# Optimization experiments

Measured on AMD Instinct MI355X. Metric: run time of the kernel, lower is better.

## Reference

```python
import jax, jax.numpy as jnp
import numpy as np

B, S, H = 2, 2048, 1024
G, HEADS = 4, 16
HPG = HEADS // G          # heads per group = 4
HD = H // HEADS           # head_dim = 64
DG = H // G               # per-group proj dim = 256
SCALE = 1.0 / np.sqrt(HD)


def setup_inputs() -> dict:
    key = jax.random.key(0)
    ks = jax.random.split(key, 6)
    w = 0.02
    return {
        "hidden_states": jax.random.normal(ks[0], (B, S, H), dtype=jnp.float32),
        "Wq": jax.random.normal(ks[1], (G, DG, H), dtype=jnp.float32) * w,
        "bq": jnp.zeros((G, DG), dtype=jnp.float32),
        "Wk": jax.random.normal(ks[2], (G, DG, H), dtype=jnp.float32) * w,
        "bk": jnp.zeros((G, DG), dtype=jnp.float32),
        "Wv": jax.random.normal(ks[3], (G, DG, H), dtype=jnp.float32) * w,
        "bv": jnp.zeros((G, DG), dtype=jnp.float32),
        "Wo": jax.random.normal(ks[4], (H, H), dtype=jnp.float32) * w,
        "bo": jnp.zeros((H,), dtype=jnp.float32),
    }


def _proj_split(x, W, b):
    # x: [B,S,H], W: [G,DG,H], b: [G,DG] -> [B,G,HPG,S,HD]
    y = jnp.einsum("bsh,gdh->bgsd", x, W) + b[None, :, None, :]
    y = y.reshape(x.shape[0], G, x.shape[1], HPG, HD)
    return jnp.transpose(y, (0, 1, 3, 2, 4))


def reference(hidden_states, Wq, bq, Wk, bk, Wv, bv, Wo, bo):
    q = _proj_split(hidden_states, Wq, bq)  # [B,G,HPG,S,HD]
    k = _proj_split(hidden_states, Wk, bk)
    v = _proj_split(hidden_states, Wv, bv)
    scores = jnp.einsum("bghqd,bghkd->bghqk", q, k) * SCALE
    attn = jax.nn.softmax(scores.astype(jnp.float32), axis=-1).astype(v.dtype)
    ctx = jnp.einsum("bghqk,bghkd->bghqd", attn, v)  # [B,G,HPG,S,HD]
    # merge: heads ordered group-major, matching torch cat over group dim
    ctx = jnp.transpose(ctx, (0, 3, 1, 2, 4)).reshape(hidden_states.shape[0], hidden_states.shape[1], H)
    return jnp.einsum("bsh,oh->bso", ctx, Wo) + bo
```

## Files before the change

### kernel.cpp

```cpp
#include <hip/hip_runtime.h>

typedef __bf16 bf16x8 __attribute__((ext_vector_type(8)));
typedef float f32x4 __attribute__((ext_vector_type(4)));
typedef float f32x16 __attribute__((ext_vector_type(16)));
typedef unsigned int uint4v __attribute__((ext_vector_type(4)));
typedef unsigned int uint2v __attribute__((ext_vector_type(2)));

#define LOG2E 1.4426950408889634f

static __device__ __forceinline__ unsigned short f2bf(float f) {
  union { float f; unsigned int u; } c; c.f = f;
  return (unsigned short)((c.u + 0x7fffu + ((c.u >> 16) & 1u)) >> 16);
}

static __device__ __forceinline__ void gload16(const void* g, void* l) {
  __builtin_amdgcn_global_load_lds(
      (const __attribute__((address_space(1))) void*)g,
      (__attribute__((address_space(3))) void*)l, 16, 0, 0);
}

static __device__ __forceinline__ float exp2fast(float x) {
#if __has_builtin(__builtin_amdgcn_exp2f)
  return __builtin_amdgcn_exp2f(x);
#else
  return exp2f(x);
#endif
}

static __device__ __forceinline__ f32x16 mfma32(bf16x8 a, bf16x8 b, f32x16 c) {
  return __builtin_amdgcn_mfma_f32_32x32x16_bf16(a, b, c, 0, 0, 0);
}

static __device__ __forceinline__ unsigned cvt_pk_bf16(float a, float b) {
  unsigned r;
  asm("v_cvt_pk_bf16_f32 %0, %1, %2" : "=v"(r) : "v"(a), "v"(b));
  return r;
}

static __device__ __forceinline__ void pl32_swap(unsigned& a, unsigned& b) {
#if __has_builtin(__builtin_amdgcn_permlane32_swap)
  uint2v r = __builtin_amdgcn_permlane32_swap(a, b, false, false);
  a = r[0]; b = r[1];
#else
  asm volatile("v_permlane32_swap_b32 %0, %1" : "+v"(a), "+v"(b));
#endif
}

__global__ void cvt_all(const float* __restrict__ x,
                        const float* __restrict__ Wq,
                        const float* __restrict__ Wk,
                        const float* __restrict__ Wv,
                        const float* __restrict__ Wo,
                        ushort4* __restrict__ dst) {
  int i = blockIdx.x * 256 + threadIdx.x;
  const float* src;
  int off;
  if (i < 1048576) {
    src = x; off = i;
  } else {
    int t = (i - 1048576) >> 18;
    off = (i - 1048576) & 262143;
    src = (t == 0) ? Wq : (t == 1) ? Wk : (t == 2) ? Wv : Wo;
  }
  float4 f = ((const float4*)src)[off];
  ushort4 o;
  o.x = f2bf(f.x); o.y = f2bf(f.y); o.z = f2bf(f.z); o.w = f2bf(f.w);
  dst[i] = o;
}

__launch_bounds__(256, 4)
__global__ void qkv_gemm(const unsigned short* __restrict__ xb,
                         const unsigned short* __restrict__ wq,
                         const unsigned short* __restrict__ wk,
                         const unsigned short* __restrict__ wv,
                         const float* __restrict__ bq,
                         const float* __restrict__ bk,
                         const float* __restrict__ bv,
                         unsigned short* __restrict__ Qo,
                         unsigned short* __restrict__ Ko,
                         unsigned short* __restrict__ VTo) {
  __shared__ unsigned short As[128 * 64];
  __shared__ unsigned short Bs[128 * 64];
  const int lg = (blockIdx.x & 7) * 96 + (blockIdx.x >> 3);
  const int s0 = (lg & 31) * 128;
  const int n0g = (lg >> 5) * 128;
  const int qkv = n0g >> 10;
  const int d0 = n0g & 1023;
  const unsigned short* W = (qkv == 0) ? wq : ((qkv == 1) ? wk : wv);
  const float* bias = (qkv == 0) ? bq : ((qkv == 1) ? bk : bv);

  const unsigned short* Aptr; const unsigned short* Bptr;
  int Aoff, Boff;
  if (qkv < 2) { Aptr = W;  Aoff = d0; Bptr = xb; Boff = s0; }
  else         { Aptr = xb; Aoff = s0; Bptr = W;  Boff = d0; }

  const int tid = threadIdx.x;
  const int lane = tid & 63;
  const int wid = tid >> 6;
  const int wm = (wid >> 1) * 64;
  const int wn = (wid & 1) * 64;
  const int lm = lane & 15;
  const int quad = lane >> 4;

  f32x4 acc[4][4] = {};

  for (int kk = 0; kk < 1024; kk += 64) {
#pragma unroll
    for (int t = 0; t < 4; ++t) {
      int i = t * 256 + tid;
      int row = i >> 3, tp = i & 7;
      int seg = tp ^ (row & 7);
      gload16(Aptr + (size_t)(Aoff + row) * 1024 + kk + seg * 8,
              As + (size_t)i * 8);
      gload16(Bptr + (size_t)(Boff + row) * 1024 + kk + seg * 8,
              Bs + (size_t)i * 8);
    }
    __syncthreads();
#pragma unroll
    for (int h = 0; h < 2; ++h) {
      bf16x8 af[4], bff[4];
#pragma unroll
      for (int mt = 0; mt < 4; ++mt) {
        int r = wm + mt * 16 + lm;
        af[mt] = *(const bf16x8*)(As + r * 64 + (((h * 4 + quad) ^ (r & 7)) * 8));
      }
#pragma unroll
      for (int nt = 0; nt < 4; ++nt) {
        int r = wn + nt * 16 + lm;
        bff[nt] = *(const bf16x8*)(Bs + r * 64 + (((h * 4 + quad) ^ (r & 7)) * 8));
      }
#pragma unroll
      for (int mt = 0; mt < 4; ++mt)
#pragma unroll
        for (int nt = 0; nt < 4; ++nt)
          acc[mt][nt] = __builtin_amdgcn_mfma_f32_16x16x32_bf16(
              af[mt], bff[nt], acc[mt][nt], 0, 0, 0);
    }
    __syncthreads();
  }

  if (qkv < 2) {
    unsigned short* OUT = (qkv == 0) ? Qo : Ko;
    const float scale = (qkv == 0) ? (0.125f * LOG2E) : 1.0f;
#pragma unroll
    for (int mt = 0; mt < 4; ++mt) {
      const int d = d0 + wm + mt * 16 + quad * 4;
      const int g = d >> 8, hpg = (d >> 6) & 3, hd = d & 63;
      const float4 bb = *(const float4*)(bias + d);
#pragma unroll
      for (int nt = 0; nt < 4; ++nt) {
        const int srow = s0 + wn + nt * 16 + lm;
        const int bidx = srow >> 11, s = srow & 2047;
        const int head = (bidx * 4 + g) * 4 + hpg;
        ushort4 o;
        o.x = f2bf((acc[mt][nt][0] + bb.x) * scale);
        o.y = f2bf((acc[mt][nt][1] + bb.y) * scale);
        o.z = f2bf((acc[mt][nt][2] + bb.z) * scale);
        o.w = f2bf((acc[mt][nt][3] + bb.w) * scale);
        *(ushort4*)(OUT + (size_t)head * 131072 + (size_t)s * 64 + hd) = o;
      }
    }
  } else {
#pragma unroll
    for (int nt = 0; nt < 4; ++nt) {
      const int d = d0 + wn + nt * 16 + lm;
      const int g = d >> 8, hpg = (d >> 6) & 3, hd = d & 63;
      const float bb = bias[d];
#pragma unroll
      for (int mt = 0; mt < 4; ++mt) {
        const int sbase = s0 + wm + mt * 16 + quad * 4;
        const int bidx = sbase >> 11, s = sbase & 2047;
        const int head = (bidx * 4 + g) * 4 + hpg;
        ushort4 o;
        o.x = f2bf(acc[mt][nt][0] + bb);
        o.y = f2bf(acc[mt][nt][1] + bb);
        o.z = f2bf(acc[mt][nt][2] + bb);
        o.w = f2bf(acc[mt][nt][3] + bb);
        *(ushort4*)(VTo + (size_t)head * 131072 + (size_t)hd * 2048 + s) = o;
      }
    }
  }
}

static __device__ __forceinline__ void stage_kv(
    const unsigned short* Kh, const unsigned short* Vh, int kv0,
    unsigned short* ksl, unsigned short* vsl, int tid) {
#pragma unroll
  for (int t = 0; t < 4; ++t) {
    int i = t * 256 + tid;
    int r = i >> 3, j = i & 7;
    gload16(Kh + (size_t)(kv0 + r) * 64 + ((j ^ (r & 7)) << 3),
            ksl + (size_t)i * 8);
  }
#pragma unroll
  for (int t = 0; t < 4; ++t) {
    int i = t * 256 + tid;
    int r = i >> 4, j = i & 15;
    gload16(Vh + (size_t)r * 2048 + kv0 + ((j ^ (r & 15)) << 3),
            vsl + (size_t)i * 8);
  }
}

__launch_bounds__(256, 2)
__global__ void attn_kernel(const unsigned short* __restrict__ Q,
                            const unsigned short* __restrict__ K,
                            const unsigned short* __restrict__ VT,
                            unsigned short* __restrict__ ctx) {
  __shared__ __align__(16) unsigned char smem[65536];

  const int f = blockIdx.x;
  const int xcd = f & 7;
  const int idx = f >> 3;
  const int head = xcd * 4 + (idx & 3);
  const int q0 = (idx >> 2) * 128;
  const int b = head >> 4;
  const int colbase = (head & 15) * 64;

  const unsigned short* Qh = Q + (size_t)head * 131072;
  const unsigned short* Kh = K + (size_t)head * 131072;
  const unsigned short* Vh = VT + (size_t)head * 131072;

  const int tid = threadIdx.x;
  const int lane = tid & 63;
  const int w = tid >> 6;
  const int wq = w & 1;
  const int wkv = w >> 1;
  const int l31 = lane & 31;
  const int hi = lane >> 5;

  stage_kv(Kh, Vh, 0, (unsigned short*)smem,
           (unsigned short*)(smem + 32768), tid);

  bf16x8 qf[2][4];
#pragma unroll
  for (int qs = 0; qs < 2; ++qs) {
    const size_t qrow = (size_t)(q0 + wq * 64 + qs * 32 + l31);
#pragma unroll
    for (int s = 0; s < 4; ++s)
      qf[qs][s] = *(const bf16x8*)(Qh + qrow * 64 + s * 16 + hi * 8);
  }

  int koff[2][4];
#pragma unroll
  for (int kb = 0; kb < 2; ++kb) {
    const int row = wkv * 64 + kb * 32 + l31;
#pragma unroll
    for (int s = 0; s < 4; ++s) {
      const int c = s * 2 + hi;
      koff[kb][s] = row * 64 + ((c ^ (row & 7)) << 3);
    }
  }
  int voff[2][2][2];
#pragma unroll
  for (int kb = 0; kb < 2; ++kb)
#pragma unroll
    for (int db = 0; db < 2; ++db) {
      const int row = db * 32 + l31;
#pragma unroll
      for (int t = 0; t < 2; ++t) {
        const int c = wkv * 8 + kb * 4 + t * 2 + hi;
        voff[kb][db][t] = row * 128 + ((c ^ (row & 15)) << 3);
      }
    }

  __syncthreads();

  float psum[2] = {0.f, 0.f};
  f32x16 oacc[2][2] = {};

  for (int it = 0; it < 16; ++it) {
    const int buf = it & 1;
    const unsigned short* kbuf = (const unsigned short*)(smem + buf * 16384);
    const unsigned short* vbuf =
        (const unsigned short*)(smem + 32768 + buf * 16384);
    if (it < 15)
      stage_kv(Kh, Vh, (it + 1) * 128,
               (unsigned short*)(smem + (buf ^ 1) * 16384),
               (unsigned short*)(smem + 32768 + (buf ^ 1) * 16384), tid);

#pragma unroll
    for (int kb = 0; kb < 2; ++kb) {
      bf16x8 kf[4], vf[2][2];
#pragma unroll
      for (int s = 0; s < 4; ++s)
        kf[s] = *(const bf16x8*)(kbuf + koff[kb][s]);
#pragma unroll
      for (int db = 0; db < 2; ++db)
#pragma unroll
        for (int t = 0; t < 2; ++t)
          vf[db][t] = *(const bf16x8*)(vbuf + voff[kb][db][t]);

#pragma unroll
      for (int qs = 0; qs < 2; ++qs) {
        f32x16 sc = {};
#pragma unroll
        for (int s = 0; s < 4; ++s)
          sc = mfma32(kf[s], qf[qs][s], sc);

        float e[16];
#pragma unroll
        for (int r = 0; r < 16; ++r) e[r] = exp2fast(sc[r]);
        {
          float t0 = (e[0] + e[1]) + (e[2] + e[3]);
          float t1 = (e[4] + e[5]) + (e[6] + e[7]);
          float t2 = (e[8] + e[9]) + (e[10] + e[11]);
          float t3 = (e[12] + e[13]) + (e[14] + e[15]);
          psum[qs] += (t0 + t1) + (t2 + t3);
        }
        unsigned p[8];
#pragma unroll
        for (int j = 0; j < 8; ++j) p[j] = cvt_pk_bf16(e[2 * j], e[2 * j + 1]);
        pl32_swap(p[0], p[2]); pl32_swap(p[1], p[3]);
        pl32_swap(p[4], p[6]); pl32_swap(p[5], p[7]);
        uint4v u0 = {p[0], p[1], p[2], p[3]};
        uint4v u1 = {p[4], p[5], p[6], p[7]};
        const bf16x8 B0 = __builtin_bit_cast(bf16x8, u0);
        const bf16x8 B1 = __builtin_bit_cast(bf16x8, u1);
#pragma unroll
        for (int db = 0; db < 2; ++db) {
          oacc[qs][db] = mfma32(vf[db][0], B0, oacc[qs][db]);
          oacc[qs][db] = mfma32(vf[db][1], B1, oacc[qs][db]);
        }
      }
    }
    __syncthreads();
  }

#pragma unroll
  for (int qs = 0; qs < 2; ++qs)
    psum[qs] += __shfl_xor(psum[qs], 32, 64);

  float* red = (float*)smem;
  float* psred = (float*)(smem + 34816);
  if (wkv == 1) {
#pragma unroll
    for (int qs = 0; qs < 2; ++qs) {
      const int qi = wq * 64 + qs * 32 + l31;
      if (hi == 0) psred[qi] = psum[qs];
#pragma unroll
      for (int db = 0; db < 2; ++db)
#pragma unroll
        for (int g = 0; g < 4; ++g) {
          f32x4 ov;
          ov[0] = oacc[qs][db][4 * g + 0];
          ov[1] = oacc[qs][db][4 * g + 1];
          ov[2] = oacc[qs][db][4 * g + 2];
          ov[3] = oacc[qs][db][4 * g + 3];
          *(f32x4*)(red + qi * 68 + db * 32 + g * 8 + hi * 4) = ov;
        }
    }
  }
  __syncthreads();
  if (wkv == 0) {
#pragma unroll
    for (int qs = 0; qs < 2; ++qs) {
      const int qi = wq * 64 + qs * 32 + l31;
      const float inv = 1.0f / (psum[qs] + psred[qi]);
      const size_t row = (size_t)(b * 2048 + q0 + qi);
#pragma unroll
      for (int db = 0; db < 2; ++db)
#pragma unroll
        for (int g = 0; g < 4; ++g) {
          f32x4 o = *(const f32x4*)(red + qi * 68 + db * 32 + g * 8 + hi * 4);
          ushort4 st;
          st.x = f2bf((o[0] + oacc[qs][db][4 * g + 0]) * inv);
          st.y = f2bf((o[1] + oacc[qs][db][4 * g + 1]) * inv);
          st.z = f2bf((o[2] + oacc[qs][db][4 * g + 2]) * inv);
          st.w = f2bf((o[3] + oacc[qs][db][4 * g + 3]) * inv);
          *(ushort4*)(ctx + row * 1024 + colbase + db * 32 + g * 8 + hi * 4) =
              st;
        }
    }
  }
}

__launch_bounds__(256, 4)
__global__ void out_gemm(const unsigned short* __restrict__ A,
                         const unsigned short* __restrict__ Wb,
                         const float* __restrict__ bo,
                         float* __restrict__ out) {
  __shared__ unsigned short As[128 * 64];
  __shared__ unsigned short Bs[64 * 64];
  const int s0 = blockIdx.x * 64;
  const int o0 = blockIdx.y * 128;

  const int tid = threadIdx.x;
  const int lane = tid & 63;
  const int wid = tid >> 6;
  const int wm = (wid >> 1) * 64;
  const int wn = (wid & 1) * 32;
  const int lm = lane & 15;
  const int quad = lane >> 4;

  f32x4 acc[4][2] = {};

  for (int kk = 0; kk < 1024; kk += 64) {
#pragma unroll
    for (int t = 0; t < 4; ++t) {
      int i = t * 256 + tid;
      int row = i >> 3, tp = i & 7;
      int seg = tp ^ (row & 7);
      gload16(Wb + (size_t)(o0 + row) * 1024 + kk + seg * 8, As + (size_t)i * 8);
    }
#pragma unroll
    for (int t = 0; t < 2; ++t) {
      int i = t * 256 + tid;
      int row = i >> 3, tp = i & 7;
      int seg = tp ^ (row & 7);
      gload16(A + (size_t)(s0 + row) * 1024 + kk + seg * 8, Bs + (size_t)i * 8);
    }
    __syncthreads();
#pragma unroll
    for (int h = 0; h < 2; ++h) {
      bf16x8 af[4], bff[2];
#pragma unroll
      for (int mt = 0; mt < 4; ++mt) {
        int r = wm + mt * 16 + lm;
        af[mt] = *(const bf16x8*)(As + r * 64 + (((h * 4 + quad) ^ (r & 7)) * 8));
      }
#pragma unroll
      for (int nt = 0; nt < 2; ++nt) {
        int r = wn + nt * 16 + lm;
        bff[nt] = *(const bf16x8*)(Bs + r * 64 + (((h * 4 + quad) ^ (r & 7)) * 8));
      }
#pragma unroll
      for (int mt = 0; mt < 4; ++mt)
#pragma unroll
        for (int nt = 0; nt < 2; ++nt)
          acc[mt][nt] = __builtin_amdgcn_mfma_f32_16x16x32_bf16(
              af[mt], bff[nt], acc[mt][nt], 0, 0, 0);
    }
    __syncthreads();
  }

#pragma unroll
  for (int mt = 0; mt < 4; ++mt) {
    const int o = o0 + wm + mt * 16 + quad * 4;
    const float4 bb = *(const float4*)(bo + o);
#pragma unroll
    for (int nt = 0; nt < 2; ++nt) {
      const int s = s0 + wn + nt * 16 + lm;
      float4 v;
      v.x = acc[mt][nt][0] + bb.x;
      v.y = acc[mt][nt][1] + bb.y;
      v.z = acc[mt][nt][2] + bb.z;
      v.w = acc[mt][nt][3] + bb.w;
      *(float4*)(out + (size_t)s * 1024 + o) = v;
    }
  }
}

extern "C" void kernel_launch(void* const* d_in, const int* in_sizes, int n_in,
                              void* d_out, int out_size, void* d_ws, size_t ws_size,
                              hipStream_t stream) {
  const float* x  = (const float*)d_in[0];
  const float* Wq = (const float*)d_in[1];
  const float* bq = (const float*)d_in[2];
  const float* Wk = (const float*)d_in[3];
  const float* bk = (const float*)d_in[4];
  const float* Wv = (const float*)d_in[5];
  const float* bv = (const float*)d_in[6];
  const float* Wo = (const float*)d_in[7];
  const float* bo = (const float*)d_in[8];
  float* out = (float*)d_out;

  char* ws = (char*)d_ws;
  unsigned short* xb  = (unsigned short*)(ws + 0);
  unsigned short* wqb = (unsigned short*)(ws + 8388608);
  unsigned short* wkb = (unsigned short*)(ws + 10485760);
  unsigned short* wvb = (unsigned short*)(ws + 12582912);
  unsigned short* wob = (unsigned short*)(ws + 14680064);
  unsigned short* Qb  = (unsigned short*)(ws + 16777216);
  unsigned short* Kb  = (unsigned short*)(ws + 25165824);
  unsigned short* VTb = (unsigned short*)(ws + 33554432);
  unsigned short* ctxb= (unsigned short*)(ws + 41943040);
  if (ws_size < 50331648) return;

  cvt_all<<<8192, 256, 0, stream>>>(x, Wq, Wk, Wv, Wo, (ushort4*)ws);
  qkv_gemm<<<dim3(768), 256, 0, stream>>>(xb, wqb, wkb, wvb, bq, bk, bv,
                                          Qb, Kb, VTb);
  attn_kernel<<<dim3(512), 256, 0, stream>>>(Qb, Kb, VTb, ctxb);
  out_gemm<<<dim3(64, 8), 256, 0, stream>>>(ctxb, wob, bo, out);
}
```

Measured before the change: 176.7 us.

## Triple-buffer K tiles with prefetch distance two and partial vmcnt waits

Splits K/V staging so K tiles are prefetched two iterations ahead in a rotating triple buffer while V stays double-buffered. The full __syncthreads is replaced by a partial s_waitcnt vmcnt plus raw s_barrier, so the most recent loads can stay in flight across the barrier. The aim is to hide more global-to-LDS latency behind the MFMA work. LDS use rises from 64KB to 80KB, which may cut occupancy below the 2 blocks per CU the launch bounds ask for. The hand-counted vmcnt values also have to match the number of outstanding loads exactly.

```diff
diff --git a/kernel.cpp b/kernel.cpp
--- a/kernel.cpp
+++ b/kernel.cpp
@@ -182,9 +182,8 @@
   }
 }
 
-static __device__ __forceinline__ void stage_kv(
-    const unsigned short* Kh, const unsigned short* Vh, int kv0,
-    unsigned short* ksl, unsigned short* vsl, int tid) {
+static __device__ __forceinline__ void stage_k(const unsigned short* Kh, int kv0,
+                                               unsigned short* ksl, int tid) {
 #pragma unroll
   for (int t = 0; t < 4; ++t) {
     int i = t * 256 + tid;
@@ -192,6 +191,9 @@
     gload16(Kh + (size_t)(kv0 + r) * 64 + ((j ^ (r & 7)) << 3),
             ksl + (size_t)i * 8);
   }
+}
+static __device__ __forceinline__ void stage_v(const unsigned short* Vh, int kv0,
+                                               unsigned short* vsl, int tid) {
 #pragma unroll
   for (int t = 0; t < 4; ++t) {
     int i = t * 256 + tid;
@@ -206,7 +208,7 @@
                             const unsigned short* __restrict__ K,
                             const unsigned short* __restrict__ VT,
                             unsigned short* __restrict__ ctx) {
-  __shared__ __align__(16) unsigned char smem[65536];
+  __shared__ __align__(16) unsigned char smem[81920];
 
   const int f = blockIdx.x;
   const int xcd = f & 7;
@@ -228,8 +230,12 @@
   const int l31 = lane & 31;
   const int hi = lane >> 5;
 
-  stage_kv(Kh, Vh, 0, (unsigned short*)smem,
-           (unsigned short*)(smem + 32768), tid);
+  unsigned short* kbA = (unsigned short*)smem;
+  unsigned short* kbB = (unsigned short*)(smem + 16384);
+  unsigned short* kbC = (unsigned short*)(smem + 32768);
+
+  stage_k(Kh, 0, kbA, tid);
+  stage_v(Vh, 0, (unsigned short*)(smem + 49152), tid);
 
   bf16x8 qf[2][4];
 #pragma unroll
@@ -263,20 +269,23 @@
       }
     }
 
-  __syncthreads();
+  stage_k(Kh, 128, kbB, tid);
+  asm volatile("s_waitcnt vmcnt(4)" ::: "memory");
+  __builtin_amdgcn_s_barrier();
+  asm volatile("" ::: "memory");
 
   float psum[2] = {0.f, 0.f};
   f32x16 oacc[2][2] = {};
 
   for (int it = 0; it < 16; ++it) {
-    const int buf = it & 1;
-    const unsigned short* kbuf = (const unsigned short*)(smem + buf * 16384);
+    const unsigned short* kbuf = kbA;
     const unsigned short* vbuf =
-        (const unsigned short*)(smem + 32768 + buf * 16384);
+        (const unsigned short*)(smem + 49152 + (it & 1) * 16384);
     if (it < 15)
-      stage_kv(Kh, Vh, (it + 1) * 128,
-               (unsigned short*)(smem + (buf ^ 1) * 16384),
-               (unsigned short*)(smem + 32768 + (buf ^ 1) * 16384), tid);
+      stage_v(Vh, (it + 1) * 128,
+              (unsigned short*)(smem + 49152 + ((it + 1) & 1) * 16384), tid);
+    if (it < 14)
+      stage_k(Kh, (it + 2) * 128, kbC, tid);
 
 #pragma unroll
     for (int kb = 0; kb < 2; ++kb) {
@@ -323,8 +332,17 @@
         }
       }
     }
-    __syncthreads();
-  }
+
+    if (it < 15) {
+      if (it < 14) asm volatile("s_waitcnt vmcnt(4)" ::: "memory");
+      else         asm volatile("s_waitcnt vmcnt(0)" ::: "memory");
+      __builtin_amdgcn_s_barrier();
+      asm volatile("" ::: "memory");
+    }
+    unsigned short* tmp = kbA; kbA = kbB; kbB = kbC; kbC = tmp;
+  }
+
+  __syncthreads();
 
 #pragma unroll
   for (int qs = 0; qs < 2; ++qs)
```

New measurement: 179.2 us. No clear change (+1.4%).
